# Kernel tuning notes

Measured on AMD Instinct MI355X. Metric: run time of the kernel, lower is better.

## Reference

```python
import jax, jax.numpy as jnp
import numpy as np

N_NODES = 20000
N_EDGES = 320000
N_ADJ = 4
D = 256
CSTR = [0, 1]          # constrained adjacency subset for the last step
RATIO = 1.0
LN_EPS = 1e-5


def setup_inputs() -> dict:
    key = jax.random.key(0)
    ks = jax.random.split(key, 10)
    x = jax.random.normal(ks[0], (N_NODES, D), dtype=jnp.float32)
    rows = jax.random.randint(ks[1], (N_ADJ, N_EDGES), 0, N_NODES)
    cols = jax.random.randint(ks[2], (N_ADJ, N_EDGES), 0, N_NODES)
    vals = jax.random.uniform(ks[3], (N_ADJ, N_EDGES), dtype=jnp.float32)
    W = jax.random.normal(ks[4], (D, D), dtype=jnp.float32) * (1.0 / np.sqrt(D))
    b = jax.random.normal(ks[5], (D,), dtype=jnp.float32) * 0.02
    ws_seq_0 = jax.random.uniform(ks[6], (2, N_ADJ - 1), dtype=jnp.float32)
    ws_seq_1 = jax.random.uniform(ks[7], (len(CSTR),), dtype=jnp.float32)
    ws_res_0 = jax.random.uniform(ks[8], (1, N_ADJ), dtype=jnp.float32)
    ws_res_1 = jax.random.uniform(ks[9], (2, len(CSTR) + 1), dtype=jnp.float32)
    return {"x": x, "rows": rows, "cols": cols, "vals": vals, "W": W, "b": b,
            "ws_seq_0": ws_seq_0, "ws_seq_1": ws_seq_1,
            "ws_res_0": ws_res_0, "ws_res_1": ws_res_1}


def reference(x, rows, cols, vals, W, b, ws_seq_0, ws_seq_1, ws_res_0, ws_res_1):
    n_nodes = x.shape[0]

    def spmm(a, h):
        # sparse [n,n] @ h : gather source features, scale, scatter-add by row
        return jax.ops.segment_sum(vals[a][:, None] * h[cols[a]], rows[a],
                                   num_segments=n_nodes)

    def op(h, adj_ids, w):
        # Op with k=1: random.sample selects ALL operators -> weighted mean
        acc = w[0] * spmm(adj_ids[0], h)
        for j, a in enumerate(adj_ids[1:], start=1):
            acc = acc + w[j] * spmm(a, h)
        return acc / len(adj_ids)

    h = x @ W + b                      # affine: [n_nodes, D]
    states = [h]
    # step i=0: seq only (res sum over states[:0] is empty -> 0), edge == 1
    s1 = op(states[0], [0, 1, 2], ws_seq_0[0])          # adjs[:-1]
    states.append(s1)
    # step i=1: seq on states[1] over adjs[:-1], res on states[0] over all adjs
    s2 = op(states[1], [0, 1, 2], ws_seq_0[1]) + RATIO * op(states[0], [0, 1, 2, 3], ws_res_0[0])
    states.append(s2)
    # last step: cstr adjacencies for seq; cstr + last adj for residuals
    out_seq = op(states[2], CSTR, ws_seq_1)
    res_ids = CSTR + [N_ADJ - 1]
    out_res = op(states[0], res_ids, ws_res_1[0]) + op(states[1], res_ids, ws_res_1[1])
    out = out_seq + RATIO * out_res
    # LayerNorm without affine params
    mu = jnp.mean(out, axis=-1, keepdims=True)
    var = jnp.var(out, axis=-1, keepdims=True)
    out = (out - mu) * jax.lax.rsqrt(var + LN_EPS)
    return jax.nn.gelu(out, approximate=False)
```

## Files before the change

kernel.cpp:

```cpp
#include <hip/hip_runtime.h>
#include <hip/hip_bf16.h>

#define N_NODES 20000
#define N_EDGES 320000
#define N_ADJ   4
#define D       256
#define DH      128
#define RPA     20004

#define NBUCK   79
#define NGRP    40
#define EPB     8000
#define GCAP    192
#define BMAX    4736

typedef __attribute__((ext_vector_type(8))) short bf8;
typedef __attribute__((ext_vector_type(4))) float f4;


__device__ __forceinline__ unsigned f2bf_bits(float x) {
    unsigned u = __float_as_uint(x);
    return (u + 0x7FFFu + ((u >> 16) & 1u)) >> 16;
}
__device__ __forceinline__ unsigned pack_bf2(float lo, float hi) {
    return f2bf_bits(lo) | (f2bf_bits(hi) << 16);
}
__device__ __forceinline__ float bf_lo(unsigned p) { return __uint_as_float(p << 16); }
__device__ __forceinline__ float bf_hi(unsigned p) { return __uint_as_float(p & 0xFFFF0000u); }


__global__ __launch_bounds__(1024) void append_kernel(const int* __restrict__ rows,
                                                      const int* __restrict__ cols,
                                                      const float* __restrict__ vals,
                                                      int* __restrict__ cnt,
                                                      uint2* __restrict__ stage) {
    __shared__ int lcnt[NBUCK];
    int g = blockIdx.x, a = blockIdx.y, t = threadIdx.x;
    if (t < NBUCK) lcnt[t] = 0;
    __syncthreads();
    int e0 = g * EPB;
    #pragma unroll 1
    for (int i = 0; i < EPB; i += 1024) {
        int e = e0 + i + t;
        if (i + t < EPB) {
            int r   = rows[a * N_EDGES + e];
            int c   = cols[a * N_EDGES + e];
            float v = vals[a * N_EDGES + e];
            int b   = r >> 8;
            int idx = atomicAdd(&lcnt[b], 1);
            if (idx < GCAP) {
                stage[(size_t)((a * NBUCK + b) * NGRP + g) * GCAP + idx] =
                    make_uint2((f2bf_bits(v) << 16) | (unsigned)c, (unsigned)(r & 255));
            }
        }
    }
    __syncthreads();
    if (t < NBUCK) cnt[(a * NBUCK + t) * NGRP + g] = min(lcnt[t], GCAP);
}


__global__ __launch_bounds__(128) void bscan_kernel(const int* __restrict__ cnt,
                                                    int* __restrict__ bbase) {
    int a = blockIdx.x, t = threadIdx.x;
    __shared__ int buf[128];
    int tot = 0;
    if (t < NBUCK) {
        for (int g = 0; g < NGRP; ++g) tot += cnt[(a * NBUCK + t) * NGRP + g];
    }
    buf[t] = tot;
    __syncthreads();
    for (int off = 1; off < 128; off <<= 1) {
        int add = (t >= off) ? buf[t - off] : 0;
        __syncthreads();
        buf[t] += add;
        __syncthreads();
    }
    if (t < NBUCK) bbase[a * 80 + t] = buf[t] - tot;
}


__global__ __launch_bounds__(256) void bsort_kernel(const int* __restrict__ cnt,
                                                    const int* __restrict__ bbase,
                                                    const uint2* __restrict__ stage,
                                                    unsigned* __restrict__ csr,
                                                    int* __restrict__ row_ptr) {
    __shared__ uint2 recs[BMAX];
    __shared__ int scn[256];
    __shared__ int offs[256];
    int b = blockIdx.x, a = blockIdx.y, t = threadIdx.x;

    int goff = 0;
    #pragma unroll 1
    for (int g = 0; g < NGRP; ++g) {
        int c = cnt[(a * NBUCK + b) * NGRP + g];
        const uint2* src = stage + (size_t)((a * NBUCK + b) * NGRP + g) * GCAP;
        for (int i = t; i < c; i += 256) {
            int d = goff + i;
            if (d < BMAX) recs[d] = src[i];
        }
        goff += c;
    }
    int total = min(goff, BMAX);

    scn[t] = 0;
    offs[t] = 0;
    __syncthreads();
    for (int i = t; i < total; i += 256) atomicAdd(&scn[recs[i].y], 1);
    __syncthreads();
    int mycnt = scn[t];
    for (int off = 1; off < 256; off <<= 1) {
        int add = (t >= off) ? scn[t - off] : 0;
        __syncthreads();
        scn[t] += add;
        __syncthreads();
    }
    int excl = scn[t] - mycnt;
    __syncthreads();
    scn[t] = excl;
    __syncthreads();

    int gbase = bbase[a * 80 + b];
    for (int i = t; i < total; i += 256) {
        int lr  = recs[i].y;
        int pos = scn[lr] + atomicAdd(&offs[lr], 1);
        csr[(size_t)a * N_EDGES + gbase + pos] = recs[i].x;
    }
    int r = b * 256 + t;
    if (r <= N_NODES) row_ptr[(size_t)a * RPA + r] = gbase + excl;
}


__global__ __launch_bounds__(256) void wfrag_kernel(const float* __restrict__ W,
                                                    uint4* __restrict__ wh,
                                                    uint4* __restrict__ wl) {
    int g = blockIdx.x * 256 + threadIdx.x;
    int lane = g & 63;
    int tile = g >> 6;
    int ks = tile >> 4, n = tile & 15;
    int m = lane & 15, quad = lane >> 4;
    int col = n * 16 + m;
    int k0  = ks * 32 + quad * 8;
    unsigned hbits[8], lbits[8];
    #pragma unroll
    for (int j = 0; j < 8; ++j) {
        float v = W[(k0 + j) * D + col];
        unsigned hb = f2bf_bits(v);
        float lo = v - __uint_as_float(hb << 16);
        hbits[j] = hb;
        lbits[j] = f2bf_bits(lo);
    }
    uint4 hh, ll;
    hh.x = hbits[0] | (hbits[1] << 16); hh.y = hbits[2] | (hbits[3] << 16);
    hh.z = hbits[4] | (hbits[5] << 16); hh.w = hbits[6] | (hbits[7] << 16);
    ll.x = lbits[0] | (lbits[1] << 16); ll.y = lbits[2] | (lbits[3] << 16);
    ll.z = lbits[4] | (lbits[5] << 16); ll.w = lbits[6] | (lbits[7] << 16);
    wh[g] = hh;
    wl[g] = ll;
}


__global__ __launch_bounds__(256) void mfma_matmul_kernel(const float* __restrict__ x,
                                                          const uint4* __restrict__ wh,
                                                          const uint4* __restrict__ wl,
                                                          const float* __restrict__ b,
                                                          unsigned* __restrict__ hp) {
    int t = threadIdx.x, wid = t >> 6, lane = t & 63;
    int r0 = blockIdx.x * 16;
    int m = lane & 15, quad = lane >> 4;

    const float* xr = x + (size_t)(r0 + m) * D + quad * 8;
    bf8 ah[8], al[8];
    #pragma unroll
    for (int ks = 0; ks < 8; ++ks) {
        float4 v0 = *(const float4*)(xr + ks * 32);
        float4 v1 = *(const float4*)(xr + ks * 32 + 4);
        float xs[8] = {v0.x, v0.y, v0.z, v0.w, v1.x, v1.y, v1.z, v1.w};
        #pragma unroll
        for (int j = 0; j < 8; ++j) {
            unsigned hb = f2bf_bits(xs[j]);
            float lo = xs[j] - __uint_as_float(hb << 16);
            ah[ks][j] = (short)hb;
            al[ks][j] = (short)f2bf_bits(lo);
        }
    }

    #pragma unroll
    for (int i = 0; i < 4; ++i) {
        int n = wid * 4 + i;
        f4 c = {0.f, 0.f, 0.f, 0.f};
        #pragma unroll
        for (int ks = 0; ks < 8; ++ks) {
            uint4 bh4 = wh[(ks * 16 + n) * 64 + lane];
            uint4 bl4 = wl[(ks * 16 + n) * 64 + lane];
            bf8 bh = *(bf8*)&bh4;
            bf8 bl = *(bf8*)&bl4;
            c = __builtin_amdgcn_mfma_f32_16x16x32_bf16(ah[ks], bh, c, 0, 0, 0);
            c = __builtin_amdgcn_mfma_f32_16x16x32_bf16(al[ks], bh, c, 0, 0, 0);
            c = __builtin_amdgcn_mfma_f32_16x16x32_bf16(ah[ks], bl, c, 0, 0, 0);
        }
        int col = n * 16 + m;
        float bb = b[col];
        #pragma unroll
        for (int reg = 0; reg < 4; ++reg) {
            float v = c[reg] + bb;
            float o = __shfl_xor(v, 1, 64);
            if ((m & 1) == 0) {
                hp[(r0 + quad * 4 + reg) * DH + (col >> 1)] = pack_bf2(v, o);
            }
        }
    }
}


__device__ __forceinline__ void gather_seg(const unsigned* __restrict__ E, int beg, int end,
                                           const uint2* __restrict__ feat2, int lane,
                                           float* __restrict__ s ) {
    int n = end - beg;
    const unsigned* e = E + beg;
    int m8 = n & ~7;
    if (m8) {
        unsigned rec[8];
        #pragma unroll
        for (int j = 0; j < 8; ++j) rec[j] = e[j];
        for (int i = 8; ; i += 8) {
            uint2 p[8];
            #pragma unroll
            for (int j = 0; j < 8; ++j)
                p[j] = feat2[((rec[j] & 0xFFFFu) << 6) + lane];
            bool more = i < m8;
            unsigned nrec[8];
            if (more) {
                #pragma unroll
                for (int j = 0; j < 8; ++j) nrec[j] = e[i + j];
            }
            #pragma unroll
            for (int j = 0; j < 8; ++j) {
                float v = __uint_as_float(rec[j] & 0xFFFF0000u);
                s[0] += v * bf_lo(p[j].x);
                s[1] += v * bf_hi(p[j].x);
                s[2] += v * bf_lo(p[j].y);
                s[3] += v * bf_hi(p[j].y);
            }
            if (!more) break;
            #pragma unroll
            for (int j = 0; j < 8; ++j) rec[j] = nrec[j];
        }
    }
    for (int i = m8; i < n; ++i) {
        unsigned rr = e[i];
        uint2 pp = feat2[((rr & 0xFFFFu) << 6) + lane];
        float vv = __uint_as_float(rr & 0xFFFF0000u);
        s[0] += vv * bf_lo(pp.x);
        s[1] += vv * bf_hi(pp.x);
        s[2] += vv * bf_lo(pp.y);
        s[3] += vv * bf_hi(pp.y);
    }
}


__global__ __launch_bounds__(256) void stage1_kernel(const uint2* __restrict__ hp2,
                                                     const int* __restrict__ row_ptr,
                                                     const unsigned* __restrict__ csr,
                                                     const float* __restrict__ wseq0,
                                                     const float* __restrict__ wres0,
                                                     const float* __restrict__ wres1,
                                                     uint2* __restrict__ s1p2,
                                                     uint2* __restrict__ s2p2,
                                                     float4* __restrict__ outp4) {
    int t = threadIdx.x, wid = t >> 6, lane = t & 63;
    int r = blockIdx.x * 4 + wid;
    float acc[N_ADJ][4];
    #pragma unroll
    for (int a = 0; a < N_ADJ; ++a) {
        acc[a][0] = acc[a][1] = acc[a][2] = acc[a][3] = 0.f;
        const int* rp = row_ptr + (size_t)a * RPA;
        int beg = __builtin_amdgcn_readfirstlane(rp[r]);
        int end = __builtin_amdgcn_readfirstlane(rp[r + 1]);
        gather_seg(csr + (size_t)a * N_EDGES, beg, end, hp2, lane, acc[a]);
    }
    const float third = 1.f / 3.f;
    float w0 = wseq0[0] * third, w1 = wseq0[1] * third, w2 = wseq0[2] * third;
    float q0 = wres0[0] * 0.25f, q1 = wres0[1] * 0.25f, q2 = wres0[2] * 0.25f, q3 = wres0[3] * 0.25f;
    float u0 = wres1[0] * third, u1 = wres1[1] * third, u2 = wres1[2] * third;
    float s1v[4], s2v[4], ov[4];
    #pragma unroll
    for (int j = 0; j < 4; ++j) {
        s1v[j] = w0 * acc[0][j] + w1 * acc[1][j] + w2 * acc[2][j];
        s2v[j] = q0 * acc[0][j] + q1 * acc[1][j] + q2 * acc[2][j] + q3 * acc[3][j];
        ov[j]  = u0 * acc[0][j] + u1 * acc[1][j] + u2 * acc[3][j];
    }
    int o = r * 64 + lane;
    s1p2[o]  = make_uint2(pack_bf2(s1v[0], s1v[1]), pack_bf2(s1v[2], s1v[3]));
    s2p2[o]  = make_uint2(pack_bf2(s2v[0], s2v[1]), pack_bf2(s2v[2], s2v[3]));
    outp4[o] = make_float4(ov[0], ov[1], ov[2], ov[3]);
}


__global__ __launch_bounds__(256) void stage2_kernel(const uint2* __restrict__ s1p2,
                                                     const int* __restrict__ row_ptr,
                                                     const unsigned* __restrict__ csr,
                                                     const float* __restrict__ wseq0,
                                                     const float* __restrict__ wres1,
                                                     uint2* __restrict__ s2p2,
                                                     float4* __restrict__ outp4) {
    int t = threadIdx.x, wid = t >> 6, lane = t & 63;
    int r = blockIdx.x * 4 + wid;
    float acc[N_ADJ][4];
    #pragma unroll
    for (int a = 0; a < N_ADJ; ++a) {
        acc[a][0] = acc[a][1] = acc[a][2] = acc[a][3] = 0.f;
        const int* rp = row_ptr + (size_t)a * RPA;
        int beg = __builtin_amdgcn_readfirstlane(rp[r]);
        int end = __builtin_amdgcn_readfirstlane(rp[r + 1]);
        gather_seg(csr + (size_t)a * N_EDGES, beg, end, s1p2, lane, acc[a]);
    }
    const float third = 1.f / 3.f;
    float w3 = wseq0[3] * third, w4 = wseq0[4] * third, w5 = wseq0[5] * third;
    float u3 = wres1[3] * third, u4 = wres1[4] * third, u5 = wres1[5] * third;
    int o = r * 64 + lane;
    uint2 sp = s2p2[o];
    float c0 = bf_lo(sp.x) + w3 * acc[0][0] + w4 * acc[1][0] + w5 * acc[2][0];
    float c1 = bf_hi(sp.x) + w3 * acc[0][1] + w4 * acc[1][1] + w5 * acc[2][1];
    float c2 = bf_lo(sp.y) + w3 * acc[0][2] + w4 * acc[1][2] + w5 * acc[2][2];
    float c3 = bf_hi(sp.y) + w3 * acc[0][3] + w4 * acc[1][3] + w5 * acc[2][3];
    s2p2[o] = make_uint2(pack_bf2(c0, c1), pack_bf2(c2, c3));
    float4 op = outp4[o];
    op.x += u3 * acc[0][0] + u4 * acc[1][0] + u5 * acc[3][0];
    op.y += u3 * acc[0][1] + u4 * acc[1][1] + u5 * acc[3][1];
    op.z += u3 * acc[0][2] + u4 * acc[1][2] + u5 * acc[3][2];
    op.w += u3 * acc[0][3] + u4 * acc[1][3] + u5 * acc[3][3];
    outp4[o] = op;
}


__global__ __launch_bounds__(256) void stage3_kernel(const uint2* __restrict__ s2p2,
                                                     const int* __restrict__ row_ptr,
                                                     const unsigned* __restrict__ csr,
                                                     const float* __restrict__ wseq1,
                                                     float4* __restrict__ outp4) {
    int t = threadIdx.x, wid = t >> 6, lane = t & 63;
    int r = blockIdx.x * 4 + wid;
    float acc[2][4];
    #pragma unroll
    for (int a = 0; a < 2; ++a) {
        acc[a][0] = acc[a][1] = acc[a][2] = acc[a][3] = 0.f;
        const int* rp = row_ptr + (size_t)a * RPA;
        int beg = __builtin_amdgcn_readfirstlane(rp[r]);
        int end = __builtin_amdgcn_readfirstlane(rp[r + 1]);
        gather_seg(csr + (size_t)a * N_EDGES, beg, end, s2p2, lane, acc[a]);
    }
    float e0 = wseq1[0] * 0.5f, e1 = wseq1[1] * 0.5f;
    int o = r * 64 + lane;
    float4 op = outp4[o];
    float v0 = op.x + e0 * acc[0][0] + e1 * acc[1][0];
    float v1 = op.y + e0 * acc[0][1] + e1 * acc[1][1];
    float v2 = op.z + e0 * acc[0][2] + e1 * acc[1][2];
    float v3 = op.w + e0 * acc[0][3] + e1 * acc[1][3];

    float sv = v0 + v1 + v2 + v3;
    float sq = v0 * v0 + v1 * v1 + v2 * v2 + v3 * v3;
    #pragma unroll
    for (int off = 32; off > 0; off >>= 1) {
        sv += __shfl_xor(sv, off, 64);
        sq += __shfl_xor(sq, off, 64);
    }
    float mu   = sv * (1.f / 256.f);
    float var  = sq * (1.f / 256.f) - mu * mu;
    float rstd = rsqrtf(var + 1e-5f);
    float y0 = (v0 - mu) * rstd;
    float y1 = (v1 - mu) * rstd;
    float y2 = (v2 - mu) * rstd;
    float y3 = (v3 - mu) * rstd;
    const float is2 = 0.70710678118654752440f;
    outp4[o] = make_float4(0.5f * y0 * (1.f + erff(y0 * is2)),
                           0.5f * y1 * (1.f + erff(y1 * is2)),
                           0.5f * y2 * (1.f + erff(y2 * is2)),
                           0.5f * y3 * (1.f + erff(y3 * is2)));
}


extern "C" void kernel_launch(void* const* d_in, const int* in_sizes, int n_in,
                              void* d_out, int out_size, void* d_ws, size_t ws_size,
                              hipStream_t stream) {
    const float* x     = (const float*)d_in[0];
    const int*   rows  = (const int*)d_in[1];
    const int*   cols  = (const int*)d_in[2];
    const float* vals  = (const float*)d_in[3];
    const float* W     = (const float*)d_in[4];
    const float* b     = (const float*)d_in[5];
    const float* wseq0 = (const float*)d_in[6];
    const float* wseq1 = (const float*)d_in[7];
    const float* wres0 = (const float*)d_in[8];
    const float* wres1 = (const float*)d_in[9];
    float4* outp4 = (float4*)d_out;

    char* p = (char*)d_ws;
    unsigned* hp  = (unsigned*)p; p += (size_t)N_NODES * DH * 4;
    unsigned* s1p = (unsigned*)p; p += (size_t)N_NODES * DH * 4;
    unsigned* s2p = (unsigned*)p; p += (size_t)N_NODES * DH * 4;
    int* row_ptr  = (int*)p;      p += (size_t)N_ADJ * RPA * 4;
    int* cnt      = (int*)p;      p += (N_ADJ * NBUCK * NGRP * 4 + 127) / 128 * 128;
    int* bbase    = (int*)p;      p += N_ADJ * 80 * 4;
    uint4* wh     = (uint4*)p;    p += 8192 * 16;
    uint4* wl     = (uint4*)p;    p += 8192 * 16;
    unsigned* csr = (unsigned*)p;
    uint2* stage  = (uint2*)s1p;

    append_kernel<<<dim3(NGRP, N_ADJ), 1024, 0, stream>>>(rows, cols, vals, cnt, stage);
    bscan_kernel<<<N_ADJ, 128, 0, stream>>>(cnt, bbase);
    bsort_kernel<<<dim3(NBUCK, N_ADJ), 256, 0, stream>>>(cnt, bbase, stage, csr, row_ptr);

    wfrag_kernel<<<32, 256, 0, stream>>>(W, wh, wl);
    mfma_matmul_kernel<<<1250, 256, 0, stream>>>(x, wh, wl, b, hp);

    stage1_kernel<<<N_NODES / 4, 256, 0, stream>>>((const uint2*)hp, row_ptr, csr,
                                                   wseq0, wres0, wres1,
                                                   (uint2*)s1p, (uint2*)s2p, outp4);
    stage2_kernel<<<N_NODES / 4, 256, 0, stream>>>((const uint2*)s1p, row_ptr, csr,
                                                   wseq0, wres1, (uint2*)s2p, outp4);
    stage3_kernel<<<N_NODES / 4, 256, 0, stream>>>((const uint2*)s2p, row_ptr, csr,
                                                   wseq1, outp4);
}
```

Measured before the change: 330.7 us.

## Merge preprocessing kernels and co-schedule matmul with CSR bucket sort

The W fragment conversion moves into extra blocks of the edge-append kernel. The bucket-scan kernel is replaced by each sort block summing its own prefix of counts. The bucket sort and the MFMA matmul are merged into one launch that dispatches on block index. This cuts five launches to two and lets the matmul and sort blocks share the GPU. The cost is redundant prefix reads in every sort block and larger shared-memory allocation for the matmul blocks, which may reduce their occupancy.

```diff
diff --git a/kernel.cpp b/kernel.cpp
--- a/kernel.cpp
+++ b/kernel.cpp
@@ -13,6 +13,7 @@
 #define EPB     8000
 #define GCAP    192
 #define BMAX    4736
+#define MMBLK   1250
 
 typedef __attribute__((ext_vector_type(8))) short bf8;
 typedef __attribute__((ext_vector_type(4))) float f4;
@@ -29,13 +30,46 @@
 __device__ __forceinline__ float bf_hi(unsigned p) { return __uint_as_float(p & 0xFFFF0000u); }
 
 
-__global__ __launch_bounds__(1024) void append_kernel(const int* __restrict__ rows,
-                                                      const int* __restrict__ cols,
-                                                      const float* __restrict__ vals,
-                                                      int* __restrict__ cnt,
-                                                      uint2* __restrict__ stage) {
+__global__ __launch_bounds__(1024) void prep_kernel(const int* __restrict__ rows,
+                                                    const int* __restrict__ cols,
+                                                    const float* __restrict__ vals,
+                                                    int* __restrict__ cnt,
+                                                    uint2* __restrict__ stage,
+                                                    const float* __restrict__ W,
+                                                    uint4* __restrict__ wh,
+                                                    uint4* __restrict__ wl) {
     __shared__ int lcnt[NBUCK];
     int g = blockIdx.x, a = blockIdx.y, t = threadIdx.x;
+
+    if (g >= NGRP) {
+        if (a != 0) return;
+        for (int i = (g - NGRP) * 1024 + t; i < 8192; i += 2048) {
+            int lane = i & 63;
+            int tile = i >> 6;
+            int ks = tile >> 4, n = tile & 15;
+            int m = lane & 15, quad = lane >> 4;
+            int col = n * 16 + m;
+            int k0  = ks * 32 + quad * 8;
+            unsigned hbits[8], lbits[8];
+            #pragma unroll
+            for (int j = 0; j < 8; ++j) {
+                float v = W[(k0 + j) * D + col];
+                unsigned hb = f2bf_bits(v);
+                float lo = v - __uint_as_float(hb << 16);
+                hbits[j] = hb;
+                lbits[j] = f2bf_bits(lo);
+            }
+            uint4 hh, ll;
+            hh.x = hbits[0] | (hbits[1] << 16); hh.y = hbits[2] | (hbits[3] << 16);
+            hh.z = hbits[4] | (hbits[5] << 16); hh.w = hbits[6] | (hbits[7] << 16);
+            ll.x = lbits[0] | (lbits[1] << 16); ll.y = lbits[2] | (lbits[3] << 16);
+            ll.z = lbits[4] | (lbits[5] << 16); ll.w = lbits[6] | (lbits[7] << 16);
+            wh[i] = hh;
+            wl[i] = ll;
+        }
+        return;
+    }
+
     if (t < NBUCK) lcnt[t] = 0;
     __syncthreads();
     int e0 = g * EPB;
@@ -59,35 +93,80 @@
 }
 
 
-__global__ __launch_bounds__(128) void bscan_kernel(const int* __restrict__ cnt,
-                                                    int* __restrict__ bbase) {
-    int a = blockIdx.x, t = threadIdx.x;
-    __shared__ int buf[128];
-    int tot = 0;
-    if (t < NBUCK) {
-        for (int g = 0; g < NGRP; ++g) tot += cnt[(a * NBUCK + t) * NGRP + g];
-    }
-    buf[t] = tot;
-    __syncthreads();
-    for (int off = 1; off < 128; off <<= 1) {
-        int add = (t >= off) ? buf[t - off] : 0;
-        __syncthreads();
-        buf[t] += add;
-        __syncthreads();
-    }
-    if (t < NBUCK) bbase[a * 80 + t] = buf[t] - tot;
-}
-
-
-__global__ __launch_bounds__(256) void bsort_kernel(const int* __restrict__ cnt,
-                                                    const int* __restrict__ bbase,
-                                                    const uint2* __restrict__ stage,
-                                                    unsigned* __restrict__ csr,
-                                                    int* __restrict__ row_ptr) {
+__global__ __launch_bounds__(256) void buildmm_kernel(const float* __restrict__ x,
+                                                      const uint4* __restrict__ wh,
+                                                      const uint4* __restrict__ wl,
+                                                      const float* __restrict__ bvec,
+                                                      unsigned* __restrict__ hp,
+                                                      const int* __restrict__ cnt,
+                                                      const uint2* __restrict__ stage,
+                                                      unsigned* __restrict__ csr,
+                                                      int* __restrict__ row_ptr) {
     __shared__ uint2 recs[BMAX];
     __shared__ int scn[256];
     __shared__ int offs[256];
-    int b = blockIdx.x, a = blockIdx.y, t = threadIdx.x;
+    __shared__ int gbase_s;
+    int t = threadIdx.x;
+
+    if (blockIdx.x < MMBLK) {
+        int wid = t >> 6, lane = t & 63;
+        int r0 = blockIdx.x * 16;
+        int m = lane & 15, quad = lane >> 4;
+
+        const float* xr = x + (size_t)(r0 + m) * D + quad * 8;
+        bf8 ah[8], al[8];
+        #pragma unroll
+        for (int ks = 0; ks < 8; ++ks) {
+            float4 v0 = *(const float4*)(xr + ks * 32);
+            float4 v1 = *(const float4*)(xr + ks * 32 + 4);
+            float xs[8] = {v0.x, v0.y, v0.z, v0.w, v1.x, v1.y, v1.z, v1.w};
+            #pragma unroll
+            for (int j = 0; j < 8; ++j) {
+                unsigned hb = f2bf_bits(xs[j]);
+                float lo = xs[j] - __uint_as_float(hb << 16);
+                ah[ks][j] = (short)hb;
+                al[ks][j] = (short)f2bf_bits(lo);
+            }
+        }
+
+        #pragma unroll
+        for (int i = 0; i < 4; ++i) {
+            int n = wid * 4 + i;
+            f4 c = {0.f, 0.f, 0.f, 0.f};
+            #pragma unroll
+            for (int ks = 0; ks < 8; ++ks) {
+                uint4 bh4 = wh[(ks * 16 + n) * 64 + lane];
+                uint4 bl4 = wl[(ks * 16 + n) * 64 + lane];
+                bf8 bh = *(bf8*)&bh4;
+                bf8 bl = *(bf8*)&bl4;
+                c = __builtin_amdgcn_mfma_f32_16x16x32_bf16(ah[ks], bh, c, 0, 0, 0);
+                c = __builtin_amdgcn_mfma_f32_16x16x32_bf16(al[ks], bh, c, 0, 0, 0);
+                c = __builtin_amdgcn_mfma_f32_16x16x32_bf16(ah[ks], bl, c, 0, 0, 0);
+            }
+            int col = n * 16 + m;
+            float bb = bvec[col];
+            #pragma unroll
+            for (int reg = 0; reg < 4; ++reg) {
+                float v = c[reg] + bb;
+                float o = __shfl_xor(v, 1, 64);
+                if ((m & 1) == 0) {
+                    hp[(r0 + quad * 4 + reg) * DH + (col >> 1)] = pack_bf2(v, o);
+                }
+            }
+        }
+        return;
+    }
+
+    int linear = blockIdx.x - MMBLK;
+    int a = linear / NBUCK, b = linear % NBUCK;
+
+    if (t == 0) gbase_s = 0;
+    __syncthreads();
+    int part = 0;
+    for (int i = t; i < b * NGRP; i += 256) part += cnt[a * (NBUCK * NGRP) + i];
+    #pragma unroll
+    for (int off = 32; off > 0; off >>= 1) part += __shfl_xor(part, off, 64);
+    if ((t & 63) == 0) atomicAdd(&gbase_s, part);
 
     int goff = 0;
     #pragma unroll 1
@@ -119,7 +198,7 @@
     scn[t] = excl;
     __syncthreads();
 
-    int gbase = bbase[a * 80 + b];
+    int gbase = gbase_s;
     for (int i = t; i < total; i += 256) {
         int lr  = recs[i].y;
         int pos = scn[lr] + atomicAdd(&offs[lr], 1);
@@ -127,88 +206,6 @@
     }
     int r = b * 256 + t;
     if (r <= N_NODES) row_ptr[(size_t)a * RPA + r] = gbase + excl;
-}
-
-
-__global__ __launch_bounds__(256) void wfrag_kernel(const float* __restrict__ W,
-                                                    uint4* __restrict__ wh,
-                                                    uint4* __restrict__ wl) {
-    int g = blockIdx.x * 256 + threadIdx.x;
-    int lane = g & 63;
-    int tile = g >> 6;
-    int ks = tile >> 4, n = tile & 15;
-    int m = lane & 15, quad = lane >> 4;
-    int col = n * 16 + m;
-    int k0  = ks * 32 + quad * 8;
-    unsigned hbits[8], lbits[8];
-    #pragma unroll
-    for (int j = 0; j < 8; ++j) {
-        float v = W[(k0 + j) * D + col];
-        unsigned hb = f2bf_bits(v);
-        float lo = v - __uint_as_float(hb << 16);
-        hbits[j] = hb;
-        lbits[j] = f2bf_bits(lo);
-    }
-    uint4 hh, ll;
-    hh.x = hbits[0] | (hbits[1] << 16); hh.y = hbits[2] | (hbits[3] << 16);
-    hh.z = hbits[4] | (hbits[5] << 16); hh.w = hbits[6] | (hbits[7] << 16);
-    ll.x = lbits[0] | (lbits[1] << 16); ll.y = lbits[2] | (lbits[3] << 16);
-    ll.z = lbits[4] | (lbits[5] << 16); ll.w = lbits[6] | (lbits[7] << 16);
-    wh[g] = hh;
-    wl[g] = ll;
-}
-
-
-__global__ __launch_bounds__(256) void mfma_matmul_kernel(const float* __restrict__ x,
-                                                          const uint4* __restrict__ wh,
-                                                          const uint4* __restrict__ wl,
-                                                          const float* __restrict__ b,
-                                                          unsigned* __restrict__ hp) {
-    int t = threadIdx.x, wid = t >> 6, lane = t & 63;
-    int r0 = blockIdx.x * 16;
-    int m = lane & 15, quad = lane >> 4;
-
-    const float* xr = x + (size_t)(r0 + m) * D + quad * 8;
-    bf8 ah[8], al[8];
-    #pragma unroll
-    for (int ks = 0; ks < 8; ++ks) {
-        float4 v0 = *(const float4*)(xr + ks * 32);
-        float4 v1 = *(const float4*)(xr + ks * 32 + 4);
-        float xs[8] = {v0.x, v0.y, v0.z, v0.w, v1.x, v1.y, v1.z, v1.w};
-        #pragma unroll
-        for (int j = 0; j < 8; ++j) {
-            unsigned hb = f2bf_bits(xs[j]);
-            float lo = xs[j] - __uint_as_float(hb << 16);
-            ah[ks][j] = (short)hb;
-            al[ks][j] = (short)f2bf_bits(lo);
-        }
-    }
-
-    #pragma unroll
-    for (int i = 0; i < 4; ++i) {
-        int n = wid * 4 + i;
-        f4 c = {0.f, 0.f, 0.f, 0.f};
-        #pragma unroll
-        for (int ks = 0; ks < 8; ++ks) {
-            uint4 bh4 = wh[(ks * 16 + n) * 64 + lane];
-            uint4 bl4 = wl[(ks * 16 + n) * 64 + lane];
-            bf8 bh = *(bf8*)&bh4;
-            bf8 bl = *(bf8*)&bl4;
-            c = __builtin_amdgcn_mfma_f32_16x16x32_bf16(ah[ks], bh, c, 0, 0, 0);
-            c = __builtin_amdgcn_mfma_f32_16x16x32_bf16(al[ks], bh, c, 0, 0, 0);
-            c = __builtin_amdgcn_mfma_f32_16x16x32_bf16(ah[ks], bl, c, 0, 0, 0);
-        }
-        int col = n * 16 + m;
-        float bb = b[col];
-        #pragma unroll
-        for (int reg = 0; reg < 4; ++reg) {
-            float v = c[reg] + bb;
-            float o = __shfl_xor(v, 1, 64);
-            if ((m & 1) == 0) {
-                hp[(r0 + quad * 4 + reg) * DH + (col >> 1)] = pack_bf2(v, o);
-            }
-        }
-    }
 }
 
 
@@ -400,18 +397,15 @@
     unsigned* s2p = (unsigned*)p; p += (size_t)N_NODES * DH * 4;
     int* row_ptr  = (int*)p;      p += (size_t)N_ADJ * RPA * 4;
     int* cnt      = (int*)p;      p += (N_ADJ * NBUCK * NGRP * 4 + 127) / 128 * 128;
-    int* bbase    = (int*)p;      p += N_ADJ * 80 * 4;
     uint4* wh     = (uint4*)p;    p += 8192 * 16;
     uint4* wl     = (uint4*)p;    p += 8192 * 16;
     unsigned* csr = (unsigned*)p;
     uint2* stage  = (uint2*)s1p;
 
-    append_kernel<<<dim3(NGRP, N_ADJ), 1024, 0, stream>>>(rows, cols, vals, cnt, stage);
-    bscan_kernel<<<N_ADJ, 128, 0, stream>>>(cnt, bbase);
-    bsort_kernel<<<dim3(NBUCK, N_ADJ), 256, 0, stream>>>(cnt, bbase, stage, csr, row_ptr);
-
-    wfrag_kernel<<<32, 256, 0, stream>>>(W, wh, wl);
-    mfma_matmul_kernel<<<1250, 256, 0, stream>>>(x, wh, wl, b, hp);
+    prep_kernel<<<dim3(NGRP + 2, N_ADJ), 1024, 0, stream>>>(rows, cols, vals, cnt,
+                                                            stage, W, wh, wl);
+    buildmm_kernel<<<MMBLK + NBUCK * N_ADJ, 256, 0, stream>>>(x, wh, wl, b, hp,
+                                                              cnt, stage, csr, row_ptr);
 
     stage1_kernel<<<N_NODES / 4, 256, 0, stream>>>((const uint2*)hp, row_ptr, csr,
                                                    wseq0, wres0, wres1,
```

Result: faster. 323.8 us (-2.1%).
